# Kernel optimization log

Hardware: AMD Instinct MI355X
Metric: run time of the kernel (lower is better)

Reference implementation:

```python
import jax, jax.numpy as jnp
import numpy as np

B, S, H, NH = 4, 2048, 1024, 16
D = H // NH  # head_dim = 64


def setup_inputs() -> dict:
    key = jax.random.key(0)
    ks = jax.random.split(key, 8)
    hidden_states = jax.random.normal(ks[0], (B, S, H), dtype=jnp.float32)
    attention_mask = jnp.zeros((B, 1, 1, S), dtype=jnp.float32)  # additive, bidirectional
    # RoPE tables (cos/sin per position, full head_dim)
    inv_freq = 1.0 / (10000.0 ** (jnp.arange(0, D, 2, dtype=jnp.float32) / D))
    t = jnp.arange(S, dtype=jnp.float32)
    freqs = jnp.outer(t, inv_freq)              # [S, D/2]
    emb = jnp.concatenate([freqs, freqs], -1)   # [S, D]
    cos, sin = jnp.cos(emb), jnp.sin(emb)
    scale = 1.0 / np.sqrt(H)
    Wq = jax.random.normal(ks[1], (H, H), dtype=jnp.float32) * scale
    Wk = jax.random.normal(ks[2], (H, H), dtype=jnp.float32) * scale
    Wv = jax.random.normal(ks[3], (H, H), dtype=jnp.float32) * scale
    Wo = jax.random.normal(ks[4], (H, H), dtype=jnp.float32) * scale
    return {"hidden_states": hidden_states, "attention_mask": attention_mask,
            "cos": cos, "sin": sin, "Wq": Wq, "Wk": Wk, "Wv": Wv, "Wo": Wo}


def _rotate_half(x):
    x1, x2 = jnp.split(x, 2, axis=-1)
    return jnp.concatenate([-x2, x1], axis=-1)


def _rope(x, cos, sin):
    # x: [B, NH, S, D]; cos/sin: [S, D]
    c = cos[None, None, :, :]
    s = sin[None, None, :, :]
    return x * c + _rotate_half(x) * s


def reference(hidden_states, attention_mask, cos, sin, Wq, Wk, Wv, Wo):
    b, s, h = hidden_states.shape
    # QKV projections (torch Linear: x @ W^T)
    def proj(W):
        y = jnp.einsum('bsh,oh->bso', hidden_states, W)
        return y.reshape(b, s, NH, D).transpose(0, 2, 1, 3)  # [B, NH, S, D]
    q, k, v = proj(Wq), proj(Wk), proj(Wv)
    q = _rope(q, cos, sin)
    k = _rope(k, cos, sin)
    scale = D ** -0.5
    scores = jnp.einsum('bhqd,bhkd->bhqk', q, k) * scale + attention_mask
    attn = jax.nn.softmax(scores, axis=-1)
    out = jnp.einsum('bhqk,bhkd->bhqd', attn, v)            # [B, NH, S, D]
    out = out.transpose(0, 2, 1, 3).reshape(b, s, h)        # [B, S, H]
    return jnp.einsum('bsh,oh->bso', out, Wo)
```

## Files before the change

### kernel.cpp

```cpp
#include <hip/hip_runtime.h>


typedef __bf16 bf16x8 __attribute__((ext_vector_type(8)));
typedef float f32x4 __attribute__((ext_vector_type(4)));
typedef float f32x16 __attribute__((ext_vector_type(16)));
typedef unsigned short u16x8 __attribute__((ext_vector_type(8)));
typedef unsigned short u16x4 __attribute__((ext_vector_type(4)));
typedef const __attribute__((address_space(1))) void* gptr_t;
typedef __attribute__((address_space(3))) void* lptr_t;

template <int N> struct ic { static constexpr int v = N; };

__device__ __forceinline__ unsigned short f2bf(float f) {
  union { float f; unsigned u; } v; v.f = f;
  unsigned r = (v.u + 0x7fffu + ((v.u >> 16) & 1u)) >> 16;
  return (unsigned short)r;
}

__device__ __forceinline__ unsigned short f2bfn(float f) {
  union { __bf16 h; unsigned short u; } v;
  v.h = (__bf16)f;
  return v.u;
}

__device__ __forceinline__ unsigned cvtpk(float lo, float hi_) {
  unsigned r;
  asm("v_cvt_pk_bf16_f32 %0, %1, %2" : "=v"(r) : "v"(lo), "v"(hi_));
  return r;
}

__device__ __forceinline__ void gld16(const void* g, void* l) {
  __builtin_amdgcn_global_load_lds((gptr_t)g, (lptr_t)l, 16, 0, 0);
}

__global__ __launch_bounds__(256) void cvt_all(
    const float* __restrict__ hidden, const float* __restrict__ Wq,
    const float* __restrict__ Wk, const float* __restrict__ Wv,
    const float* __restrict__ Wo, unsigned short* __restrict__ Xb,
    unsigned short* __restrict__ Wb) {
  size_t i8 = ((size_t)blockIdx.x * 256 + threadIdx.x) * 8;
  const float* src;
  unsigned short* dst;
  if (i8 < 8388608) {
    src = hidden + i8;
    dst = Xb + i8;
  } else {
    size_t r = i8 - 8388608;
    int wsel = (int)(r >> 20);
    size_t off = r & 1048575;
    const float* wsrc = (wsel == 0) ? Wq : (wsel == 1) ? Wk : (wsel == 2) ? Wv : Wo;
    src = wsrc + off;
    dst = Wb + r;
  }
  f32x4 a = *(const f32x4*)(src);
  f32x4 b = *(const f32x4*)(src + 4);
  u16x8 o;
  o[0] = f2bf(a[0]); o[1] = f2bf(a[1]); o[2] = f2bf(a[2]); o[3] = f2bf(a[3]);
  o[4] = f2bf(b[0]); o[5] = f2bf(b[1]); o[6] = f2bf(b[2]); o[7] = f2bf(b[3]);
  *(u16x8*)dst = o;
}

__global__ __launch_bounds__(768, 3) void gemm_qkv(
    const unsigned short* __restrict__ A,
    const unsigned short* __restrict__ W0, const unsigned short* __restrict__ W1,
    const unsigned short* __restrict__ W2,
    const float* __restrict__ cosT, const float* __restrict__ sinT,
    unsigned short* __restrict__ Qh, unsigned short* __restrict__ Kh,
    unsigned short* __restrict__ Vh) {
  __shared__ char sm[65536];
  const int tid = threadIdx.x, lane = tid & 63, w = tid >> 6;
  const int l15 = lane & 15, h2 = lane >> 4;
  const int z = w >> 2, sub = w & 3;
  const int wm = sub >> 1, wn = sub & 1;
  const int brow = blockIdx.y * 128;
  const int bcol = blockIdx.x * 128;

  const char* Abase = (const char*)A + (size_t)brow * 2048;
  const char* Wb0 = (const char*)W0 + (size_t)bcol * 2048;
  const char* Wb1 = (const char*)W1 + (size_t)bcol * 2048;
  const char* Wb2 = (const char*)W2 + (size_t)bcol * 2048;

  const char* gsrc[6];
  int gdst[6];
#pragma unroll
  for (int i = 0; i < 6; ++i) {
    int g = tid + i * 768;
    bool val = g < 4096;
    int gg = val ? g : 0;
    int r = (gg & 1023) >> 3;
    int sw = ((gg & 7) * 16) ^ ((r & 7) << 4);
    const char* base;
    if (gg < 1024) base = Abase;
    else {
      int zz = (gg >> 10) - 1;
      base = (zz == 0) ? Wb0 : (zz == 1 ? Wb1 : Wb2);
    }
    gsrc[i] = val ? (base + (size_t)r * 2048 + sw) : nullptr;
    gdst[i] = gg * 16;
  }

  f32x4 acc[4][4];
#pragma unroll
  for (int m = 0; m < 4; ++m)
#pragma unroll
    for (int n = 0; n < 4; ++n) acc[m][n] = (f32x4){0.f, 0.f, 0.f, 0.f};

  const char* Asw = sm;
  const char* Bsw = sm + 16384 + z * 16384;

  for (int kt = 0; kt < 16; ++kt) {
#pragma unroll
    for (int i = 0; i < 6; ++i)
      if (gsrc[i]) gld16(gsrc[i] + kt * 128, sm + gdst[i]);
    __syncthreads();
#pragma unroll
    for (int kk = 0; kk < 2; ++kk) {
      int kb = kk * 64 + h2 * 16;
      bf16x8 af[4], bfr[4];
#pragma unroll
      for (int m = 0; m < 4; ++m) {
        int r = wm * 64 + m * 16 + l15;
        af[m] = *(const bf16x8*)(Asw + r * 128 + (kb ^ ((r & 7) << 4)));
      }
#pragma unroll
      for (int n = 0; n < 4; ++n) {
        int r = wn * 64 + n * 16 + l15;
        bfr[n] = *(const bf16x8*)(Bsw + r * 128 + (kb ^ ((r & 7) << 4)));
      }
#pragma unroll
      for (int m = 0; m < 4; ++m)
#pragma unroll
        for (int n = 0; n < 4; ++n)
          acc[m][n] = __builtin_amdgcn_mfma_f32_16x16x32_bf16(af[m], bfr[n],
                                                              acc[m][n], 0, 0, 0);
    }
    __syncthreads();
  }

  const int h = blockIdx.x * 2 + wn;
  if (z == 2) {
#pragma unroll
    for (int m = 0; m < 4; ++m) {
      int row0 = brow + wm * 64 + m * 16 + h2 * 4;
      int b = row0 >> 11, s0 = row0 & 2047;
      size_t base = (size_t)(b * 16 + h) * 64 * 2048 + s0;
#pragma unroll
      for (int n = 0; n < 4; ++n) {
        int dl = n * 16 + l15;
        u16x4 pw;
#pragma unroll
        for (int i = 0; i < 4; ++i) pw[i] = f2bf(acc[m][n][i]);
        *(u16x4*)(Vh + base + (size_t)dl * 2048) = pw;
      }
    }
  } else {
    unsigned short* dst = (z == 0) ? Qh : Kh;
    const float qs = (z == 0) ? 0.18033688f : 1.0f;
#pragma unroll
    for (int m = 0; m < 4; ++m)
#pragma unroll
      for (int i = 0; i < 4; ++i) {
        int row = brow + wm * 64 + m * 16 + h2 * 4 + i;
        int b = row >> 11, s = row & 2047;
        size_t hb2 = ((size_t)(b * 16 + h) * 2048 + s) * 64;
#pragma unroll
        for (int n = 0; n < 2; ++n) {
          int dl = n * 16 + l15;
          float c = cosT[s * 64 + dl], sn = sinT[s * 64 + dl];
          float lo = acc[m][n][i], hi = acc[m][n + 2][i];
          dst[hb2 + dl] = f2bf((lo * c - hi * sn) * qs);
          dst[hb2 + dl + 32] = f2bf((hi * c + lo * sn) * qs);
        }
      }
  }
}

__global__ __launch_bounds__(256, 3) void gemm_k(
    const unsigned short* __restrict__ A, const unsigned short* __restrict__ W0,
    float* __restrict__ Cout) {
  __shared__ char sm[32768];
  char* As = sm;
  char* Bs = sm + 16384;
  const int tid = threadIdx.x, lane = tid & 63, w = tid >> 6;
  const int wm = w >> 1, wn = w & 1;
  const int brow = blockIdx.y * 128;
  const int bcol = blockIdx.x * 128;

  f32x4 acc[4][4];
#pragma unroll
  for (int m = 0; m < 4; ++m)
#pragma unroll
    for (int n = 0; n < 4; ++n) acc[m][n] = (f32x4){0.f, 0.f, 0.f, 0.f};

  const char* Abase = (const char*)A + (size_t)brow * 2048;
  const char* Bbase = (const char*)W0 + (size_t)bcol * 2048;

  for (int kt = 0; kt < 1024; kt += 64) {
#pragma unroll
    for (int c = 0; c < 4; ++c) {
      int Lb = w * 4096 + c * 1024;
      int L = Lb + lane * 16;
      int r = L >> 7, kb = L & 127;
      int sw = kb ^ ((r & 7) << 4);
      gld16(Abase + (size_t)r * 2048 + kt * 2 + sw, As + Lb);
      gld16(Bbase + (size_t)r * 2048 + kt * 2 + sw, Bs + Lb);
    }
    __syncthreads();
#pragma unroll
    for (int kk = 0; kk < 2; ++kk) {
      int kb = kk * 64 + (lane >> 4) * 16;
      bf16x8 af[4], bfr[4];
#pragma unroll
      for (int m = 0; m < 4; ++m) {
        int r = wm * 64 + m * 16 + (lane & 15);
        af[m] = *(const bf16x8*)(As + r * 128 + (kb ^ ((r & 7) << 4)));
      }
#pragma unroll
      for (int n = 0; n < 4; ++n) {
        int r = wn * 64 + n * 16 + (lane & 15);
        bfr[n] = *(const bf16x8*)(Bs + r * 128 + (kb ^ ((r & 7) << 4)));
      }
#pragma unroll
      for (int m = 0; m < 4; ++m)
#pragma unroll
        for (int n = 0; n < 4; ++n)
          acc[m][n] = __builtin_amdgcn_mfma_f32_16x16x32_bf16(af[m], bfr[n],
                                                              acc[m][n], 0, 0, 0);
    }
    __syncthreads();
  }

#pragma unroll
  for (int m = 0; m < 4; ++m)
#pragma unroll
    for (int n = 0; n < 4; ++n)
#pragma unroll
      for (int i = 0; i < 4; ++i) {
        int row = brow + wm * 64 + m * 16 + (lane >> 4) * 4 + i;
        int col = bcol + wn * 64 + n * 16 + (lane & 15);
        Cout[(size_t)row * 1024 + col] = acc[m][n][i];
      }
}

__global__ __launch_bounds__(256, 4) void attn_k(
    const unsigned short* __restrict__ Q, const unsigned short* __restrict__ K,
    const unsigned short* __restrict__ Vt, const float* __restrict__ mask,
    unsigned short* __restrict__ O) {
  __shared__ char Ks[2][8192];
  __shared__ char Vs[2][8192];
  __shared__ float l_arr[4][32];
  const int tid = threadIdx.x, lane = tid & 63, w = tid >> 6;
  const int q31 = lane & 31, hi = lane >> 5;
  const int wg = blockIdx.x;
  const int work = (wg & 7) * 128 + (wg >> 3);
  const int qt = work & 15, hl = work >> 4;
  const int h = hl & 15, b = hl >> 4;
  const size_t hb = (size_t)(b * 16 + h) * (2048 * 64);
  const int q0 = qt * 128 + w * 32;
  const float L2E = 1.44269504f;
  const float MREF = 12.0f;
  const int rdo = q31 * 32 + hi * 16;

  bf16x8 qb[4];
  {
    const char* qrow = (const char*)(Q + hb + (size_t)(q0 + q31) * 64);
#pragma unroll
    for (int ks = 0; ks < 4; ++ks)
      qb[ks] = *(const bf16x8*)(qrow + ks * 32 + hi * 16);
  }

  float l_part = 0.f;
  f32x16 oacc[2];
#pragma unroll
  for (int e = 0; e < 16; ++e) { oacc[0][e] = 0.f; oacc[1][e] = 0.f; }

  int koff0, koff1, vof0, vof1;
  {
    int L0 = w * 2048 + lane * 16;
    int c0 = L0 >> 12, ks0 = (L0 >> 10) & 3, q0l = (L0 >> 5) & 31,
        hi0 = (L0 >> 4) & 1;
    int row0 = c0 * 32 + q0l, kb0 = ks0 * 32 + hi0 * 16;
    koff0 = row0 * 128 + kb0;
    vof0 = row0 * 4096 + kb0;
    int L1 = L0 + 1024;
    int c1 = L1 >> 12, ks1 = (L1 >> 10) & 3, q1l = (L1 >> 5) & 31,
        hi1 = (L1 >> 4) & 1;
    int row1 = c1 * 32 + q1l, kb1 = ks1 * 32 + hi1 * 16;
    koff1 = row1 * 128 + kb1;
    vof1 = row1 * 4096 + kb1;
  }
  const char* Kg = (const char*)(K + hb);
  const char* Vg = (const char*)(Vt + hb);
  const float* mp = mask + (size_t)b * 2048;

  gld16(Kg + koff0, Ks[0] + w * 2048);
  gld16(Kg + koff1, Ks[0] + w * 2048 + 1024);
  gld16(Vg + vof0, Vs[0] + w * 2048);
  gld16(Vg + vof1, Vs[0] + w * 2048 + 1024);

  auto body = [&](auto curc, int t) {
    constexpr int cur = decltype(curc)::v;
    constexpr int nxt = 1 - cur;
    if (t < 31) {
      const char* kp = Kg + (size_t)(t + 1) * 8192;
      const char* vp = Vg + (size_t)(t + 1) * 128;
      gld16(kp + koff0, Ks[nxt] + w * 2048);
      gld16(kp + koff1, Ks[nxt] + w * 2048 + 1024);
      gld16(vp + vof0, Vs[nxt] + w * 2048);
      gld16(vp + vof1, Vs[nxt] + w * 2048 + 1024);
      asm volatile("s_waitcnt vmcnt(4)" ::: "memory");
    } else {
      asm volatile("s_waitcnt vmcnt(0)" ::: "memory");
    }
    __builtin_amdgcn_sched_barrier(0);
    __builtin_amdgcn_s_barrier();
    __builtin_amdgcn_sched_barrier(0);

    const float* mrow = mp + t * 64;

    f32x16 sacc[2];
#pragma unroll
    for (int c = 0; c < 2; ++c) {
#pragma unroll
      for (int g = 0; g < 4; ++g) {
        f32x4 mv = *(const f32x4*)(mrow + c * 32 + g * 8 + hi * 4);
#pragma unroll
        for (int i = 0; i < 4; ++i)
          sacc[c][g * 4 + i] = fmaf(mv[i], L2E, -MREF);
      }
      __builtin_amdgcn_s_setprio(1);
#pragma unroll
      for (int ks = 0; ks < 4; ++ks) {
        bf16x8 kf =
            *(const bf16x8*)(Ks[cur] + (c * 4 + ks) * 1024 + rdo);
        sacc[c] = __builtin_amdgcn_mfma_f32_32x32x16_bf16(kf, qb[ks], sacc[c],
                                                          0, 0, 0);
      }
      __builtin_amdgcn_s_setprio(0);
#pragma unroll
      for (int e = 0; e < 16; ++e)
        sacc[c][e] = __builtin_amdgcn_exp2f(sacc[c][e]);
      float s0 = (sacc[c][0] + sacc[c][1]) + (sacc[c][2] + sacc[c][3]);
      float s1 = (sacc[c][4] + sacc[c][5]) + (sacc[c][6] + sacc[c][7]);
      float s2 = (sacc[c][8] + sacc[c][9]) + (sacc[c][10] + sacc[c][11]);
      float s3 = (sacc[c][12] + sacc[c][13]) + (sacc[c][14] + sacc[c][15]);
      l_part += (s0 + s1) + (s2 + s3);
    }

    __builtin_amdgcn_s_setprio(1);
#pragma unroll
    for (int c = 0; c < 2; ++c) {
#pragma unroll
      for (int par = 0; par < 2; ++par) {
        const int t2 = c * 2 + par;
        unsigned a0 = cvtpk(sacc[c][par * 8 + 0], sacc[c][par * 8 + 1]);
        unsigned a1 = cvtpk(sacc[c][par * 8 + 2], sacc[c][par * 8 + 3]);
        unsigned b0 = cvtpk(sacc[c][par * 8 + 4], sacc[c][par * 8 + 5]);
        unsigned b1 = cvtpk(sacc[c][par * 8 + 6], sacc[c][par * 8 + 7]);
        asm("v_permlane32_swap_b32 %0, %1" : "+v"(a0), "+v"(b0));
        asm("v_permlane32_swap_b32 %0, %1" : "+v"(a1), "+v"(b1));
        union { unsigned u[4]; bf16x8 v; } pu;
        pu.u[0] = a0; pu.u[1] = a1; pu.u[2] = b0; pu.u[3] = b1;
        bf16x8 vf0 = *(const bf16x8*)(Vs[cur] + t2 * 1024 + rdo);
        bf16x8 vf1 = *(const bf16x8*)(Vs[cur] + 4096 + t2 * 1024 + rdo);
        oacc[0] = __builtin_amdgcn_mfma_f32_32x32x16_bf16(pu.v, vf0, oacc[0],
                                                          0, 0, 0);
        oacc[1] = __builtin_amdgcn_mfma_f32_32x32x16_bf16(pu.v, vf1, oacc[1],
                                                          0, 0, 0);
      }
    }
    __builtin_amdgcn_s_setprio(0);
    __builtin_amdgcn_sched_barrier(0);
    __builtin_amdgcn_s_barrier();
  };

  for (int t = 0; t < 32; t += 2) {
    body(ic<0>{}, t);
    body(ic<1>{}, t + 1);
  }

  float lr = l_part + __shfl_xor(l_part, 32, 64);
  l_arr[w][q31] = 1.0f / lr;

#pragma unroll
  for (int g = 0; g < 4; ++g) {
    f32x4 iv = *(const f32x4*)(&l_arr[w][g * 8 + hi * 4]);
    const int qrow = q0 + g * 8 + hi * 4;
#pragma unroll
    for (int i = 0; i < 4; ++i) {
      size_t rb = (size_t)(b * 2048 + qrow + i) * 1024 + h * 64;
      O[rb + q31] = f2bfn(oacc[0][g * 4 + i] * iv[i]);
      O[rb + 32 + q31] = f2bfn(oacc[1][g * 4 + i] * iv[i]);
    }
  }
}

extern "C" void kernel_launch(void* const* d_in, const int* in_sizes, int n_in,
                              void* d_out, int out_size, void* d_ws, size_t ws_size,
                              hipStream_t stream) {
  const float* hidden = (const float*)d_in[0];
  const float* amask = (const float*)d_in[1];
  const float* cosT = (const float*)d_in[2];
  const float* sinT = (const float*)d_in[3];
  const float* Wq = (const float*)d_in[4];
  const float* Wk = (const float*)d_in[5];
  const float* Wv = (const float*)d_in[6];
  const float* Wo = (const float*)d_in[7];
  float* out = (float*)d_out;

  if (ws_size < (size_t)92274688) return;
  unsigned short* Xb = (unsigned short*)d_ws;
  unsigned short* Wqb = Xb + (size_t)8192 * 1024;
  unsigned short* Wkb = Wqb + (size_t)1024 * 1024;
  unsigned short* Wvb = Wkb + (size_t)1024 * 1024;
  unsigned short* Wob = Wvb + (size_t)1024 * 1024;
  unsigned short* Qh = Wob + (size_t)1024 * 1024;
  unsigned short* Kh = Qh + (size_t)8388608;
  unsigned short* Vt = Kh + (size_t)8388608;
  unsigned short* Ob = Vt + (size_t)8388608;

  cvt_all<<<6144, 256, 0, stream>>>(hidden, Wq, Wk, Wv, Wo, Xb, Wqb);

  gemm_qkv<<<dim3(8, 64), 768, 0, stream>>>(Xb, Wqb, Wkb, Wvb, cosT, sinT, Qh,
                                            Kh, Vt);
  attn_k<<<1024, 256, 0, stream>>>(Qh, Kh, Vt, amask, Ob);
  gemm_k<<<dim3(8, 64), 256, 0, stream>>>(Ob, Wob, out);
}
```

Measured before the change: 199.6 us.

## Double-buffer LDS in QKV GEMM and remap blocks for XCD-friendly tile order

The QKV projection GEMM now uses two 64KB LDS buffers. It prefetches the next K-tile while computing the current one, using explicit vmcnt waits and raw s_barrier in place of two __syncthreads per iteration. The grid becomes 1D, and block IDs are remapped so consecutive tiles spread across XCDs, which should improve L2 reuse of A/W tiles. The intent is to hide global-to-LDS latency behind MFMA work. In exchange, doubling LDS to 128KB per block lowers how many blocks can be resident per CU.

After: 192.4 us. 3.6% less time.

```diff
diff --git a/kernel.cpp b/kernel.cpp
--- a/kernel.cpp
+++ b/kernel.cpp
@@ -67,13 +67,16 @@
     const float* __restrict__ cosT, const float* __restrict__ sinT,
     unsigned short* __restrict__ Qh, unsigned short* __restrict__ Kh,
     unsigned short* __restrict__ Vh) {
-  __shared__ char sm[65536];
+  __shared__ char sm[131072];
   const int tid = threadIdx.x, lane = tid & 63, w = tid >> 6;
   const int l15 = lane & 15, h2 = lane >> 4;
   const int z = w >> 2, sub = w & 3;
   const int wm = sub >> 1, wn = sub & 1;
-  const int brow = blockIdx.y * 128;
-  const int bcol = blockIdx.x * 128;
+  const int wg = blockIdx.x;
+  const int work = (wg & 7) * 64 + (wg >> 3);
+  const int bx = work & 7, by = work >> 3;
+  const int brow = by * 128;
+  const int bcol = bx * 128;
 
   const char* Abase = (const char*)A + (size_t)brow * 2048;
   const char* Wb0 = (const char*)W0 + (size_t)bcol * 2048;
@@ -105,14 +108,27 @@
 #pragma unroll
     for (int n = 0; n < 4; ++n) acc[m][n] = (f32x4){0.f, 0.f, 0.f, 0.f};
 
-  const char* Asw = sm;
-  const char* Bsw = sm + 16384 + z * 16384;
+#pragma unroll
+  for (int i = 0; i < 6; ++i)
+    if (gsrc[i]) gld16(gsrc[i], sm + gdst[i]);
 
   for (int kt = 0; kt < 16; ++kt) {
-#pragma unroll
-    for (int i = 0; i < 6; ++i)
-      if (gsrc[i]) gld16(gsrc[i] + kt * 128, sm + gdst[i]);
-    __syncthreads();
+    const int cur = kt & 1, nxt = cur ^ 1;
+    if (kt < 15) {
+#pragma unroll
+      for (int i = 0; i < 6; ++i)
+        if (gsrc[i]) gld16(gsrc[i] + (kt + 1) * 128, sm + nxt * 65536 + gdst[i]);
+      if (w < 4) asm volatile("s_waitcnt vmcnt(6)" ::: "memory");
+      else       asm volatile("s_waitcnt vmcnt(5)" ::: "memory");
+    } else {
+      asm volatile("s_waitcnt vmcnt(0)" ::: "memory");
+    }
+    __builtin_amdgcn_sched_barrier(0);
+    __builtin_amdgcn_s_barrier();
+    __builtin_amdgcn_sched_barrier(0);
+
+    const char* Asw = sm + cur * 65536;
+    const char* Bsw = sm + cur * 65536 + 16384 + z * 16384;
 #pragma unroll
     for (int kk = 0; kk < 2; ++kk) {
       int kb = kk * 64 + h2 * 16;
@@ -134,10 +150,11 @@
           acc[m][n] = __builtin_amdgcn_mfma_f32_16x16x32_bf16(af[m], bfr[n],
                                                               acc[m][n], 0, 0, 0);
     }
-    __syncthreads();
-  }
-
-  const int h = blockIdx.x * 2 + wn;
+    __builtin_amdgcn_sched_barrier(0);
+    __builtin_amdgcn_s_barrier();
+  }
+
+  const int h = bx * 2 + wn;
   if (z == 2) {
 #pragma unroll
     for (int m = 0; m < 4; ++m) {
@@ -421,8 +438,7 @@
 
   cvt_all<<<6144, 256, 0, stream>>>(hidden, Wq, Wk, Wv, Wo, Xb, Wqb);
 
-  gemm_qkv<<<dim3(8, 64), 768, 0, stream>>>(Xb, Wqb, Wkb, Wvb, cosT, sinT, Qh,
-                                            Kh, Vt);
+  gemm_qkv<<<512, 768, 0, stream>>>(Xb, Wqb, Wkb, Wvb, cosT, sinT, Qh, Kh, Vt);
   attn_k<<<1024, 256, 0, stream>>>(Qh, Kh, Vt, amask, Ob);
   gemm_k<<<dim3(8, 64), 256, 0, stream>>>(Ob, Wob, out);
 }
```
